# Kernel tuning notes

Hardware: AMD Instinct MI355X
Metric: run time of the kernel (lower is better)

Reference implementation:

```python
import jax, jax.numpy as jnp
import numpy as np
from jax import lax

C = 256
B, H, W = 8, 64, 64


def dwconv(x, w, b, pad):
    # x: [B,C,H,W], w: [C,1,kh,kw] depthwise (groups=C), b: [C]
    y = lax.conv_general_dilated(
        x, w,
        window_strides=(1, 1),
        padding=pad,
        dimension_numbers=('NCHW', 'OIHW', 'NCHW'),
        feature_group_count=x.shape[1],
    )
    return y + b[None, :, None, None]


def setup_inputs() -> dict:
    key = jax.random.key(0)
    ks = jax.random.split(key, 16)
    s = 0.05
    inp = {
        'x': jax.random.normal(ks[0], (B, C, H, W), jnp.float32),
        'w0':   jax.random.normal(ks[1], (C, 1, 5, 5), jnp.float32) * s,
        'b0':   jax.random.normal(ks[2], (C,), jnp.float32) * s,
        'w0_1': jax.random.normal(ks[3], (C, 1, 1, 7), jnp.float32) * s,
        'b0_1': jax.random.normal(ks[4], (C,), jnp.float32) * s,
        'w0_2': jax.random.normal(ks[5], (C, 1, 7, 1), jnp.float32) * s,
        'b0_2': jax.random.normal(ks[6], (C,), jnp.float32) * s,
        'w1_1': jax.random.normal(ks[7], (C, 1, 1, 11), jnp.float32) * s,
        'b1_1': jax.random.normal(ks[8], (C,), jnp.float32) * s,
        'w1_2': jax.random.normal(ks[9], (C, 1, 11, 1), jnp.float32) * s,
        'b1_2': jax.random.normal(ks[10], (C,), jnp.float32) * s,
        'w2_1': jax.random.normal(ks[11], (C, 1, 1, 21), jnp.float32) * s,
        'b2_1': jax.random.normal(ks[12], (C,), jnp.float32) * s,
        'w2_2': jax.random.normal(ks[13], (C, 1, 21, 1), jnp.float32) * s,
        'b2_2': jax.random.normal(ks[14], (C,), jnp.float32) * s,
    }
    return inp


def reference(x, w0, b0, w0_1, b0_1, w0_2, b0_2,
              w1_1, b1_1, w1_2, b1_2, w2_1, b2_1, w2_2, b2_2):
    # 5x5 depthwise, pad 2
    attn = dwconv(x, w0, b0, ((2, 2), (2, 2)))
    # stage 0: 1x7 / 7x1 strips
    a0x = dwconv(attn, w0_1, b0_1, ((0, 0), (3, 3)))
    a0y = dwconv(attn, w0_2, b0_2, ((3, 3), (0, 0)))
    attn_0 = a0x * a0y
    # stage 1: 1x11 / 11x1 strips
    a1x = dwconv(a0x, w1_1, b1_1, ((0, 0), (5, 5)))
    a1y = dwconv(a0y, w1_2, b1_2, ((5, 5), (0, 0)))
    attn_1 = a1x * a1y
    # stage 2: 1x21 / 21x1 strips
    a2x = dwconv(a1x, w2_1, b2_1, ((0, 0), (10, 10)))
    a2y = dwconv(a1y, w2_2, b2_2, ((10, 10), (0, 0)))
    attn_2 = a2x * a2y
    return (attn_0, attn_1, attn_2)
```

## Files before the change

### kernel.cpp

```cpp
#include <hip/hip_runtime.h>


#define RA_W 4624
#define RB_W 4352
#define LDS_WORDS (RA_W + RB_W)

typedef float v2f __attribute__((ext_vector_type(2)));

__device__ __forceinline__ float dpp_prev(float v) {
    return __int_as_float(__builtin_amdgcn_update_dpp(
        0, __float_as_int(v), 0x111, 0xF, 0xF, false));
}
__device__ __forceinline__ float dpp_next(float v) {
    return __int_as_float(__builtin_amdgcn_update_dpp(
        0, __float_as_int(v), 0x101, 0xF, 0xF, false));
}
__device__ __forceinline__ void ld4p(const float* p, v2f* w) {
    float4 q = *(const float4*)p;
    w[0].x = q.x; w[0].y = q.y; w[1].x = q.z; w[1].y = q.w;
}
__device__ __forceinline__ void st4p(float* p, v2f a, v2f b) {
    float4 q; q.x = a.x; q.y = a.y; q.z = b.x; q.w = b.y;
    *(float4*)p = q;
}
__device__ __forceinline__ float elem(const v2f* a, int e) {
    return (e & 1) ? a[e >> 1].y : a[e >> 1].x;
}

template<int K, int TAPOFF>
__device__ __forceinline__ void conv_acc(const float* __restrict__ wrow,
                                         const v2f* wnd, v2f* A) {
    #pragma unroll
    for (int v = 0; v < K; v++) {
        const float w = wrow[v];
        const int u = v + TAPOFF;
        if ((u & 1) == 0) {
            v2f wv; wv.x = w; wv.y = w;
            #pragma unroll
            for (int k = 0; k < 8; k++) A[k] += wv * wnd[(u >> 1) + k];
        } else {
            #pragma unroll
            for (int k = 0; k < 8; k++) {
                A[k].x += w * wnd[(u >> 1) + k].y;
                A[k].y += w * wnd[(u >> 1) + k + 1].x;
            }
        }
    }
}

template<int H>
__device__ __forceinline__ void build_twnd(const float* s, float* w, int jg) {
    float pv[H], nv[H];
    #pragma unroll
    for (int d = 0; d < H; d++) pv[d] = dpp_prev(s[16 - H + d]);
    #pragma unroll
    for (int d = 0; d < H; d++) nv[d] = dpp_next(s[d]);
    #pragma unroll
    for (int d = 0; d < H; d++) w[d] = jg ? pv[d] : 0.f;
    #pragma unroll
    for (int k = 0; k < 16; k++) w[H + k] = s[k];
    #pragma unroll
    for (int d = 0; d < H; d++) w[H + 16 + d] = (jg < 3) ? nv[d] : 0.f;
}
template<int K>
__device__ __forceinline__ void conv_t(const float* __restrict__ wrow,
                                       const float* w, float bb, float* acc) {
    #pragma unroll
    for (int k = 0; k < 16; k++) acc[k] = bb;
    #pragma unroll
    for (int u = 0; u < K; u++) {
        const float ww = wrow[u];
        #pragma unroll
        for (int k = 0; k < 16; k++) acc[k] += ww * w[k + u];
    }
}

__global__ __launch_bounds__(256, 4)
void msca_fused(const float* __restrict__ x,
                const float* __restrict__ w0,   const float* __restrict__ b0,
                const float* __restrict__ w0_1, const float* __restrict__ b0_1,
                const float* __restrict__ w0_2, const float* __restrict__ b0_2,
                const float* __restrict__ w1_1, const float* __restrict__ b1_1,
                const float* __restrict__ w1_2, const float* __restrict__ b1_2,
                const float* __restrict__ w2_1, const float* __restrict__ b2_1,
                const float* __restrict__ w2_2, const float* __restrict__ b2_2,
                float* __restrict__ out)
{
    __shared__ __align__(16) float lds[LDS_WORDS];
    float* RA = lds;
    float* RB = lds + RA_W;

    const int t  = threadIdx.x;
    const int r  = t >> 2;
    const int jg = t & 3;
    const int j0 = jg << 4;

    const int plane = blockIdx.x;
    const int ch    = plane & 255;

    const float* xg = x + (size_t)plane * 4096;
    float* o0 = out + (size_t)plane * 4096;
    float* o1 = o0 + 8388608;
    float* o2 = o1 + 8388608;

    v2f xR2[8];
    #pragma unroll
    for (int m = 0; m < 4; m++) ld4p(&xg[r * 64 + j0 + 4 * m], &xR2[2 * m]);

    #pragma unroll
    for (int k0 = 0; k0 < 2; k0++) {
        int k = t + 256 * k0;
        if (k < 272) RA[k < 136 ? k : k + 4352] = 0.f;
    }
    if (t < 64) {
        int b = (t + 2) * 68;
        RA[b] = 0.f; RA[b + 1] = 0.f; RA[b + 66] = 0.f; RA[b + 67] = 0.f;
    }
    {
        float* row = &RA[(r + 2) * 68];
        row[j0 + 2] = xR2[0].x;  row[j0 + 3] = xR2[0].y;
        st4p(&row[j0 + 4],  xR2[1], xR2[2]);
        st4p(&row[j0 + 8],  xR2[3], xR2[4]);
        st4p(&row[j0 + 12], xR2[5], xR2[6]);
        row[j0 + 16] = xR2[7].x; row[j0 + 17] = xR2[7].y;
    }
    __syncthreads();

    v2f attn2[8];
    {
        const float bb = b0[ch];
        #pragma unroll
        for (int k = 0; k < 8; k++) { attn2[k].x = bb; attn2[k].y = bb; }
        #pragma unroll
        for (int dr = 0; dr < 5; dr++) {
            v2f wnd[10];
            if (dr == 2) {
                float e0 = dpp_prev(xR2[7].x), e1 = dpp_prev(xR2[7].y);
                float n0 = dpp_next(xR2[0].x), n1 = dpp_next(xR2[0].y);
                wnd[0].x = jg ? e0 : 0.f;  wnd[0].y = jg ? e1 : 0.f;
                #pragma unroll
                for (int k = 0; k < 8; k++) wnd[1 + k] = xR2[k];
                wnd[9].x = (jg < 3) ? n0 : 0.f;  wnd[9].y = (jg < 3) ? n1 : 0.f;
            } else {
                const float* row = &RA[(r + dr) * 68 + j0];
                #pragma unroll
                for (int m = 0; m < 5; m++) ld4p(&row[4 * m], &wnd[2 * m]);
            }
            conv_acc<5, 0>(w0 + ch * 25 + dr * 5, wnd, attn2);
        }
        #pragma unroll
        for (int e = 0; e < 16; e++) RB[(j0 + e) * 68 + r] = elem(attn2, e);
    }
    __syncthreads();

    v2f a0x2[8];
    {
        const float bb = b0_1[ch];
        #pragma unroll
        for (int k = 0; k < 8; k++) { a0x2[k].x = bb; a0x2[k].y = bb; }
        v2f wnd[12];
        float p13 = dpp_prev(attn2[6].y), p14 = dpp_prev(attn2[7].x), p15 = dpp_prev(attn2[7].y);
        float n0 = dpp_next(attn2[0].x), n1 = dpp_next(attn2[0].y), n2 = dpp_next(attn2[1].x);
        wnd[0].x = 0.f;               wnd[0].y = jg ? p13 : 0.f;
        wnd[1].x = jg ? p14 : 0.f;    wnd[1].y = jg ? p15 : 0.f;
        #pragma unroll
        for (int k = 0; k < 8; k++) wnd[2 + k] = attn2[k];
        wnd[10].x = (jg < 3) ? n0 : 0.f;  wnd[10].y = (jg < 3) ? n1 : 0.f;
        wnd[11].x = (jg < 3) ? n2 : 0.f;  wnd[11].y = 0.f;
        conv_acc<7, 1>(w0_1 + ch * 7, wnd, a0x2);
    }
    float sT[16];
    #pragma unroll
    for (int m = 0; m < 4; m++) {
        float4 q = *(const float4*)&RB[r * 68 + j0 + 4 * m];
        sT[4 * m] = q.x; sT[4 * m + 1] = q.y; sT[4 * m + 2] = q.z; sT[4 * m + 3] = q.w;
    }
    float a0y[16];
    {
        float w[22];
        build_twnd<3>(sT, w, jg);
        conv_t<7>(w0_2 + ch * 7, w, b0_2[ch], a0y);
        #pragma unroll
        for (int e = 0; e < 16; e++) RA[(j0 + e) * 68 + r] = a0y[e];
    }
    __syncthreads();

    v2f prod0[8];
    #pragma unroll
    for (int m = 0; m < 4; m++) {
        v2f p[2]; ld4p(&RA[r * 68 + j0 + 4 * m], p);
        prod0[2 * m]     = a0x2[2 * m] * p[0];
        prod0[2 * m + 1] = a0x2[2 * m + 1] * p[1];
    }
    v2f a1x2[8];
    {
        const float bb = b1_1[ch];
        #pragma unroll
        for (int k = 0; k < 8; k++) { a1x2[k].x = bb; a1x2[k].y = bb; }
        v2f wnd[14];
        float p11 = dpp_prev(a0x2[5].y), p12 = dpp_prev(a0x2[6].x), p13 = dpp_prev(a0x2[6].y);
        float p14 = dpp_prev(a0x2[7].x), p15 = dpp_prev(a0x2[7].y);
        float n0 = dpp_next(a0x2[0].x), n1 = dpp_next(a0x2[0].y), n2 = dpp_next(a0x2[1].x);
        float n3 = dpp_next(a0x2[1].y), n4 = dpp_next(a0x2[2].x);
        wnd[0].x = 0.f;             wnd[0].y = jg ? p11 : 0.f;
        wnd[1].x = jg ? p12 : 0.f;  wnd[1].y = jg ? p13 : 0.f;
        wnd[2].x = jg ? p14 : 0.f;  wnd[2].y = jg ? p15 : 0.f;
        #pragma unroll
        for (int k = 0; k < 8; k++) wnd[3 + k] = a0x2[k];
        wnd[11].x = (jg < 3) ? n0 : 0.f;  wnd[11].y = (jg < 3) ? n1 : 0.f;
        wnd[12].x = (jg < 3) ? n2 : 0.f;  wnd[12].y = (jg < 3) ? n3 : 0.f;
        wnd[13].x = (jg < 3) ? n4 : 0.f;  wnd[13].y = 0.f;
        conv_acc<11, 1>(w1_1 + ch * 11, wnd, a1x2);
    }
    float a1y[16];
    {
        float w[26];
        build_twnd<5>(a0y, w, jg);
        conv_t<11>(w1_2 + ch * 11, w, b1_2[ch], a1y);
        #pragma unroll
        for (int e = 0; e < 16; e++) RB[(j0 + e) * 68 + r] = a1y[e];
    }
    __syncthreads();

    st4p(&o0[r * 64 + j0],      prod0[0], prod0[1]);
    st4p(&o0[r * 64 + j0 + 4],  prod0[2], prod0[3]);
    st4p(&o0[r * 64 + j0 + 8],  prod0[4], prod0[5]);
    st4p(&o0[r * 64 + j0 + 12], prod0[6], prod0[7]);

    v2f prod1[8];
    #pragma unroll
    for (int m = 0; m < 4; m++) {
        v2f p[2]; ld4p(&RB[r * 68 + j0 + 4 * m], p);
        prod1[2 * m]     = a1x2[2 * m] * p[0];
        prod1[2 * m + 1] = a1x2[2 * m + 1] * p[1];
    }
    v2f a2x2[8];
    {
        const float bb = b2_1[ch];
        #pragma unroll
        for (int k = 0; k < 8; k++) { a2x2[k].x = bb; a2x2[k].y = bb; }
        v2f wnd[18];
        float pv[10], nv[10];
        #pragma unroll
        for (int d = 0; d < 10; d++) {
            int q = 6 + d;
            float pe = dpp_prev((q & 1) ? a1x2[q >> 1].y : a1x2[q >> 1].x);
            float ne = dpp_next((d & 1) ? a1x2[d >> 1].y : a1x2[d >> 1].x);
            pv[d] = jg ? pe : 0.f;
            nv[d] = (jg < 3) ? ne : 0.f;
        }
        #pragma unroll
        for (int m = 0; m < 5; m++) { wnd[m].x = pv[2 * m]; wnd[m].y = pv[2 * m + 1]; }
        #pragma unroll
        for (int k = 0; k < 8; k++) wnd[5 + k] = a1x2[k];
        #pragma unroll
        for (int m = 0; m < 5; m++) { wnd[13 + m].x = nv[2 * m]; wnd[13 + m].y = nv[2 * m + 1]; }
        conv_acc<21, 0>(w2_1 + ch * 21, wnd, a2x2);
    }
    {
        float w[36], a2y[16];
        build_twnd<10>(a1y, w, jg);
        conv_t<21>(w2_2 + ch * 21, w, b2_2[ch], a2y);
        #pragma unroll
        for (int e = 0; e < 16; e++) RA[(j0 + e) * 68 + r] = a2y[e];
    }
    __syncthreads();

    st4p(&o1[r * 64 + j0],      prod1[0], prod1[1]);
    st4p(&o1[r * 64 + j0 + 4],  prod1[2], prod1[3]);
    st4p(&o1[r * 64 + j0 + 8],  prod1[4], prod1[5]);
    st4p(&o1[r * 64 + j0 + 12], prod1[6], prod1[7]);
    #pragma unroll
    for (int m = 0; m < 4; m++) {
        v2f p[2]; ld4p(&RA[r * 68 + j0 + 4 * m], p);
        v2f q0 = a2x2[2 * m] * p[0];
        v2f q1 = a2x2[2 * m + 1] * p[1];
        st4p(&o2[r * 64 + j0 + 4 * m], q0, q1);
    }
}

extern "C" void kernel_launch(void* const* d_in, const int* in_sizes, int n_in,
                              void* d_out, int out_size, void* d_ws, size_t ws_size,
                              hipStream_t stream) {
    msca_fused<<<2048, 256, 0, stream>>>(
        (const float*)d_in[0],
        (const float*)d_in[1],  (const float*)d_in[2],
        (const float*)d_in[3],  (const float*)d_in[4],
        (const float*)d_in[5],  (const float*)d_in[6],
        (const float*)d_in[7],  (const float*)d_in[8],
        (const float*)d_in[9],  (const float*)d_in[10],
        (const float*)d_in[11], (const float*)d_in[12],
        (const float*)d_in[13], (const float*)d_in[14],
        (float*)d_out);
}
```

Baseline: 47.22 us.

## Use 512 threads per plane with 8 columns each and swizzled LDS transposes

Each block now runs 512 threads, each owning 8 columns of a row instead of 16, which halves per-thread register state and raises the occupancy target. Horizontal strip halos are gathered with DPP row shifts by 1 and 2 lanes, since the 21-tap conv needs data from two neighbours. The transpose scatter and read now use an XOR swizzle to cut LDS bank conflicts. The packed v2f math is dropped in favour of scalar FMAs, which may give up dual-issue throughput.

After: 44.85 us. 1.05x faster.

```diff
diff --git a/kernel.cpp b/kernel.cpp
--- a/kernel.cpp
+++ b/kernel.cpp
@@ -5,77 +5,102 @@
 #define RB_W 4352
 #define LDS_WORDS (RA_W + RB_W)
 
-typedef float v2f __attribute__((ext_vector_type(2)));
-
-__device__ __forceinline__ float dpp_prev(float v) {
+__device__ __forceinline__ float dppsr1(float v) {
     return __int_as_float(__builtin_amdgcn_update_dpp(
         0, __float_as_int(v), 0x111, 0xF, 0xF, false));
 }
-__device__ __forceinline__ float dpp_next(float v) {
+__device__ __forceinline__ float dppsr2(float v) {
+    return __int_as_float(__builtin_amdgcn_update_dpp(
+        0, __float_as_int(v), 0x112, 0xF, 0xF, false));
+}
+__device__ __forceinline__ float dppsl1(float v) {
     return __int_as_float(__builtin_amdgcn_update_dpp(
         0, __float_as_int(v), 0x101, 0xF, 0xF, false));
 }
-__device__ __forceinline__ void ld4p(const float* p, v2f* w) {
-    float4 q = *(const float4*)p;
-    w[0].x = q.x; w[0].y = q.y; w[1].x = q.z; w[1].y = q.w;
-}
-__device__ __forceinline__ void st4p(float* p, v2f a, v2f b) {
-    float4 q; q.x = a.x; q.y = a.y; q.z = b.x; q.w = b.y;
-    *(float4*)p = q;
-}
-__device__ __forceinline__ float elem(const v2f* a, int e) {
-    return (e & 1) ? a[e >> 1].y : a[e >> 1].x;
-}
-
-template<int K, int TAPOFF>
-__device__ __forceinline__ void conv_acc(const float* __restrict__ wrow,
-                                         const v2f* wnd, v2f* A) {
+__device__ __forceinline__ float dppsl2(float v) {
+    return __int_as_float(__builtin_amdgcn_update_dpp(
+        0, __float_as_int(v), 0x102, 0xF, 0xF, false));
+}
+__device__ __forceinline__ void ld8(const float* p, float* d) {
+    float4 a = *(const float4*)p, b = *(const float4*)(p + 4);
+    d[0]=a.x; d[1]=a.y; d[2]=a.z; d[3]=a.w; d[4]=b.x; d[5]=b.y; d[6]=b.z; d[7]=b.w;
+}
+__device__ __forceinline__ void st8(float* p, const float* d) {
+    float4 a, b;
+    a.x=d[0]; a.y=d[1]; a.z=d[2]; a.w=d[3]; b.x=d[4]; b.y=d[5]; b.z=d[6]; b.w=d[7];
+    *(float4*)p = a; *(float4*)(p + 4) = b;
+}
+
+template<int K, int W0, int N>
+__device__ __forceinline__ void cpart(const float* __restrict__ wt,
+                                      const float* s, float* acc) {
     #pragma unroll
     for (int v = 0; v < K; v++) {
-        const float w = wrow[v];
-        const int u = v + TAPOFF;
-        if ((u & 1) == 0) {
-            v2f wv; wv.x = w; wv.y = w;
-            #pragma unroll
-            for (int k = 0; k < 8; k++) A[k] += wv * wnd[(u >> 1) + k];
-        } else {
-            #pragma unroll
-            for (int k = 0; k < 8; k++) {
-                A[k].x += w * wnd[(u >> 1) + k].y;
-                A[k].y += w * wnd[(u >> 1) + k + 1].x;
-            }
+        #pragma unroll
+        for (int j = 0; j < 8; j++) {
+            const int p = j + v - W0;
+            if (p >= 0 && p < N) acc[j] += wt[v] * s[p];
         }
     }
 }
 
 template<int H>
-__device__ __forceinline__ void build_twnd(const float* s, float* w, int jg) {
+__device__ __forceinline__ void sconv(const float* __restrict__ wt, float bb,
+                                      const float* a, bool pm, bool np, float* acc) {
+    constexpr int K = 2 * H + 1;
     float pv[H], nv[H];
     #pragma unroll
-    for (int d = 0; d < H; d++) pv[d] = dpp_prev(s[16 - H + d]);
-    #pragma unroll
-    for (int d = 0; d < H; d++) nv[d] = dpp_next(s[d]);
-    #pragma unroll
-    for (int d = 0; d < H; d++) w[d] = jg ? pv[d] : 0.f;
-    #pragma unroll
-    for (int k = 0; k < 16; k++) w[H + k] = s[k];
-    #pragma unroll
-    for (int d = 0; d < H; d++) w[H + 16 + d] = (jg < 3) ? nv[d] : 0.f;
-}
-template<int K>
-__device__ __forceinline__ void conv_t(const float* __restrict__ wrow,
-                                       const float* w, float bb, float* acc) {
-    #pragma unroll
-    for (int k = 0; k < 16; k++) acc[k] = bb;
-    #pragma unroll
-    for (int u = 0; u < K; u++) {
-        const float ww = wrow[u];
-        #pragma unroll
-        for (int k = 0; k < 16; k++) acc[k] += ww * w[k + u];
-    }
-}
-
-__global__ __launch_bounds__(256, 4)
+    for (int i = 0; i < H; i++) pv[i] = dppsr1(a[8 - H + i]);
+    #pragma unroll
+    for (int i = 0; i < H; i++) nv[i] = dppsl1(a[i]);
+    #pragma unroll
+    for (int i = 0; i < H; i++) pv[i] = pm ? pv[i] : 0.f;
+    #pragma unroll
+    for (int i = 0; i < H; i++) nv[i] = np ? nv[i] : 0.f;
+    #pragma unroll
+    for (int j = 0; j < 8; j++) acc[j] = bb;
+    cpart<K, 0, H>(wt, pv, acc);
+    cpart<K, H, 8>(wt, a, acc);
+    cpart<K, H + 8, H>(wt, nv, acc);
+}
+
+__device__ __forceinline__ void sconv21(const float* __restrict__ wt, float bb,
+                                        const float* a, bool pm, bool pm2,
+                                        bool np, bool np2, float* acc) {
+    #pragma unroll
+    for (int j = 0; j < 8; j++) acc[j] = bb;
+    {
+        float q[2];
+        q[0] = dppsr2(a[6]); q[1] = dppsr2(a[7]);
+        q[0] = pm2 ? q[0] : 0.f; q[1] = pm2 ? q[1] : 0.f;
+        cpart<21, 0, 2>(wt, q, acc);
+    }
+    {
+        float pv[8];
+        #pragma unroll
+        for (int i = 0; i < 8; i++) pv[i] = dppsr1(a[i]);
+        #pragma unroll
+        for (int i = 0; i < 8; i++) pv[i] = pm ? pv[i] : 0.f;
+        cpart<21, 2, 8>(wt, pv, acc);
+    }
+    cpart<21, 10, 8>(wt, a, acc);
+    {
+        float nv[8];
+        #pragma unroll
+        for (int i = 0; i < 8; i++) nv[i] = dppsl1(a[i]);
+        #pragma unroll
+        for (int i = 0; i < 8; i++) nv[i] = np ? nv[i] : 0.f;
+        cpart<21, 18, 8>(wt, nv, acc);
+    }
+    {
+        float q[2];
+        q[0] = dppsl2(a[0]); q[1] = dppsl2(a[1]);
+        q[0] = np2 ? q[0] : 0.f; q[1] = np2 ? q[1] : 0.f;
+        cpart<21, 26, 2>(wt, q, acc);
+    }
+}
+
+__global__ __launch_bounds__(512, 8)
 void msca_fused(const float* __restrict__ x,
                 const float* __restrict__ w0,   const float* __restrict__ b0,
                 const float* __restrict__ w0_1, const float* __restrict__ b0_1,
@@ -90,10 +115,16 @@
     float* RA = lds;
     float* RB = lds + RA_W;
 
-    const int t  = threadIdx.x;
-    const int r  = t >> 2;
-    const int jg = t & 3;
-    const int j0 = jg << 4;
+    const int t     = threadIdx.x;
+    const int maj   = t >> 3;
+    const int lane8 = t & 7;
+    const int j0    = lane8 << 3;
+
+    const bool pm  = lane8 >= 1, np  = lane8 <= 6;
+    const bool pm2 = lane8 >= 2, np2 = lane8 <= 5;
+
+    const int scat = maj ^ (lane8 << 3);
+    const int rdb  = maj * 68 + ((lane8 ^ ((maj >> 3) & 7)) << 3);
 
     const int plane = blockIdx.x;
     const int ch    = plane & 255;
@@ -103,186 +134,108 @@
     float* o1 = o0 + 8388608;
     float* o2 = o1 + 8388608;
 
-    v2f xR2[8];
-    #pragma unroll
-    for (int m = 0; m < 4; m++) ld4p(&xg[r * 64 + j0 + 4 * m], &xR2[2 * m]);
-
-    #pragma unroll
-    for (int k0 = 0; k0 < 2; k0++) {
-        int k = t + 256 * k0;
-        if (k < 272) RA[k < 136 ? k : k + 4352] = 0.f;
-    }
-    if (t < 64) {
-        int b = (t + 2) * 68;
-        RA[b] = 0.f; RA[b + 1] = 0.f; RA[b + 66] = 0.f; RA[b + 67] = 0.f;
-    }
-    {
-        float* row = &RA[(r + 2) * 68];
-        row[j0 + 2] = xR2[0].x;  row[j0 + 3] = xR2[0].y;
-        st4p(&row[j0 + 4],  xR2[1], xR2[2]);
-        st4p(&row[j0 + 8],  xR2[3], xR2[4]);
-        st4p(&row[j0 + 12], xR2[5], xR2[6]);
-        row[j0 + 16] = xR2[7].x; row[j0 + 17] = xR2[7].y;
-    }
-    __syncthreads();
-
-    v2f attn2[8];
+    float xr[8];
+    ld8(&xg[maj * 64 + j0], xr);
+    if (t < 136) { RA[t] = 0.f; RA[t + 4488] = 0.f; }
+    if (t < 256) {
+        int rr = 2 + (t >> 2), cc = t & 3;
+        RA[rr * 68 + (cc < 2 ? cc : cc + 64)] = 0.f;
+    }
+    {
+        float* row = &RA[(maj + 2) * 68 + j0 + 2];
+        float2 p;
+        p.x = xr[0]; p.y = xr[1]; ((float2*)row)[0] = p;
+        p.x = xr[2]; p.y = xr[3]; ((float2*)row)[1] = p;
+        p.x = xr[4]; p.y = xr[5]; ((float2*)row)[2] = p;
+        p.x = xr[6]; p.y = xr[7]; ((float2*)row)[3] = p;
+    }
+    __syncthreads();
+
+    float attn[8];
     {
         const float bb = b0[ch];
         #pragma unroll
-        for (int k = 0; k < 8; k++) { attn2[k].x = bb; attn2[k].y = bb; }
+        for (int j = 0; j < 8; j++) attn[j] = bb;
+        const float* w0p = w0 + ch * 25;
         #pragma unroll
         for (int dr = 0; dr < 5; dr++) {
-            v2f wnd[10];
-            if (dr == 2) {
-                float e0 = dpp_prev(xR2[7].x), e1 = dpp_prev(xR2[7].y);
-                float n0 = dpp_next(xR2[0].x), n1 = dpp_next(xR2[0].y);
-                wnd[0].x = jg ? e0 : 0.f;  wnd[0].y = jg ? e1 : 0.f;
+            float wnd[12];
+            const float* rowp = &RA[(maj + dr) * 68 + j0];
+            float4 qa = *(const float4*)rowp;
+            float4 qb = *(const float4*)(rowp + 4);
+            float4 qc = *(const float4*)(rowp + 8);
+            wnd[0]=qa.x; wnd[1]=qa.y; wnd[2]=qa.z;  wnd[3]=qa.w;
+            wnd[4]=qb.x; wnd[5]=qb.y; wnd[6]=qb.z;  wnd[7]=qb.w;
+            wnd[8]=qc.x; wnd[9]=qc.y; wnd[10]=qc.z; wnd[11]=qc.w;
+            #pragma unroll
+            for (int v = 0; v < 5; v++) {
+                const float ww = w0p[dr * 5 + v];
                 #pragma unroll
-                for (int k = 0; k < 8; k++) wnd[1 + k] = xR2[k];
-                wnd[9].x = (jg < 3) ? n0 : 0.f;  wnd[9].y = (jg < 3) ? n1 : 0.f;
-            } else {
-                const float* row = &RA[(r + dr) * 68 + j0];
-                #pragma unroll
-                for (int m = 0; m < 5; m++) ld4p(&row[4 * m], &wnd[2 * m]);
+                for (int j = 0; j < 8; j++) attn[j] += ww * wnd[j + v];
             }
-            conv_acc<5, 0>(w0 + ch * 25 + dr * 5, wnd, attn2);
         }
         #pragma unroll
-        for (int e = 0; e < 16; e++) RB[(j0 + e) * 68 + r] = elem(attn2, e);
-    }
-    __syncthreads();
-
-    v2f a0x2[8];
-    {
-        const float bb = b0_1[ch];
-        #pragma unroll
-        for (int k = 0; k < 8; k++) { a0x2[k].x = bb; a0x2[k].y = bb; }
-        v2f wnd[12];
-        float p13 = dpp_prev(attn2[6].y), p14 = dpp_prev(attn2[7].x), p15 = dpp_prev(attn2[7].y);
-        float n0 = dpp_next(attn2[0].x), n1 = dpp_next(attn2[0].y), n2 = dpp_next(attn2[1].x);
-        wnd[0].x = 0.f;               wnd[0].y = jg ? p13 : 0.f;
-        wnd[1].x = jg ? p14 : 0.f;    wnd[1].y = jg ? p15 : 0.f;
-        #pragma unroll
-        for (int k = 0; k < 8; k++) wnd[2 + k] = attn2[k];
-        wnd[10].x = (jg < 3) ? n0 : 0.f;  wnd[10].y = (jg < 3) ? n1 : 0.f;
-        wnd[11].x = (jg < 3) ? n2 : 0.f;  wnd[11].y = 0.f;
-        conv_acc<7, 1>(w0_1 + ch * 7, wnd, a0x2);
-    }
-    float sT[16];
-    #pragma unroll
-    for (int m = 0; m < 4; m++) {
-        float4 q = *(const float4*)&RB[r * 68 + j0 + 4 * m];
-        sT[4 * m] = q.x; sT[4 * m + 1] = q.y; sT[4 * m + 2] = q.z; sT[4 * m + 3] = q.w;
-    }
-    float a0y[16];
-    {
-        float w[22];
-        build_twnd<3>(sT, w, jg);
-        conv_t<7>(w0_2 + ch * 7, w, b0_2[ch], a0y);
-        #pragma unroll
-        for (int e = 0; e < 16; e++) RA[(j0 + e) * 68 + r] = a0y[e];
-    }
-    __syncthreads();
-
-    v2f prod0[8];
-    #pragma unroll
-    for (int m = 0; m < 4; m++) {
-        v2f p[2]; ld4p(&RA[r * 68 + j0 + 4 * m], p);
-        prod0[2 * m]     = a0x2[2 * m] * p[0];
-        prod0[2 * m + 1] = a0x2[2 * m + 1] * p[1];
-    }
-    v2f a1x2[8];
-    {
-        const float bb = b1_1[ch];
-        #pragma unroll
-        for (int k = 0; k < 8; k++) { a1x2[k].x = bb; a1x2[k].y = bb; }
-        v2f wnd[14];
-        float p11 = dpp_prev(a0x2[5].y), p12 = dpp_prev(a0x2[6].x), p13 = dpp_prev(a0x2[6].y);
-        float p14 = dpp_prev(a0x2[7].x), p15 = dpp_prev(a0x2[7].y);
-        float n0 = dpp_next(a0x2[0].x), n1 = dpp_next(a0x2[0].y), n2 = dpp_next(a0x2[1].x);
-        float n3 = dpp_next(a0x2[1].y), n4 = dpp_next(a0x2[2].x);
-        wnd[0].x = 0.f;             wnd[0].y = jg ? p11 : 0.f;
-        wnd[1].x = jg ? p12 : 0.f;  wnd[1].y = jg ? p13 : 0.f;
-        wnd[2].x = jg ? p14 : 0.f;  wnd[2].y = jg ? p15 : 0.f;
-        #pragma unroll
-        for (int k = 0; k < 8; k++) wnd[3 + k] = a0x2[k];
-        wnd[11].x = (jg < 3) ? n0 : 0.f;  wnd[11].y = (jg < 3) ? n1 : 0.f;
-        wnd[12].x = (jg < 3) ? n2 : 0.f;  wnd[12].y = (jg < 3) ? n3 : 0.f;
-        wnd[13].x = (jg < 3) ? n4 : 0.f;  wnd[13].y = 0.f;
-        conv_acc<11, 1>(w1_1 + ch * 11, wnd, a1x2);
-    }
-    float a1y[16];
-    {
-        float w[26];
-        build_twnd<5>(a0y, w, jg);
-        conv_t<11>(w1_2 + ch * 11, w, b1_2[ch], a1y);
-        #pragma unroll
-        for (int e = 0; e < 16; e++) RB[(j0 + e) * 68 + r] = a1y[e];
-    }
-    __syncthreads();
-
-    st4p(&o0[r * 64 + j0],      prod0[0], prod0[1]);
-    st4p(&o0[r * 64 + j0 + 4],  prod0[2], prod0[3]);
-    st4p(&o0[r * 64 + j0 + 8],  prod0[4], prod0[5]);
-    st4p(&o0[r * 64 + j0 + 12], prod0[6], prod0[7]);
-
-    v2f prod1[8];
-    #pragma unroll
-    for (int m = 0; m < 4; m++) {
-        v2f p[2]; ld4p(&RB[r * 68 + j0 + 4 * m], p);
-        prod1[2 * m]     = a1x2[2 * m] * p[0];
-        prod1[2 * m + 1] = a1x2[2 * m + 1] * p[1];
-    }
-    v2f a2x2[8];
-    {
-        const float bb = b2_1[ch];
-        #pragma unroll
-        for (int k = 0; k < 8; k++) { a2x2[k].x = bb; a2x2[k].y = bb; }
-        v2f wnd[18];
-        float pv[10], nv[10];
-        #pragma unroll
-        for (int d = 0; d < 10; d++) {
-            int q = 6 + d;
-            float pe = dpp_prev((q & 1) ? a1x2[q >> 1].y : a1x2[q >> 1].x);
-            float ne = dpp_next((d & 1) ? a1x2[d >> 1].y : a1x2[d >> 1].x);
-            pv[d] = jg ? pe : 0.f;
-            nv[d] = (jg < 3) ? ne : 0.f;
-        }
-        #pragma unroll
-        for (int m = 0; m < 5; m++) { wnd[m].x = pv[2 * m]; wnd[m].y = pv[2 * m + 1]; }
-        #pragma unroll
-        for (int k = 0; k < 8; k++) wnd[5 + k] = a1x2[k];
-        #pragma unroll
-        for (int m = 0; m < 5; m++) { wnd[13 + m].x = nv[2 * m]; wnd[13 + m].y = nv[2 * m + 1]; }
-        conv_acc<21, 0>(w2_1 + ch * 21, wnd, a2x2);
-    }
-    {
-        float w[36], a2y[16];
-        build_twnd<10>(a1y, w, jg);
-        conv_t<21>(w2_2 + ch * 21, w, b2_2[ch], a2y);
-        #pragma unroll
-        for (int e = 0; e < 16; e++) RA[(j0 + e) * 68 + r] = a2y[e];
-    }
-    __syncthreads();
-
-    st4p(&o1[r * 64 + j0],      prod1[0], prod1[1]);
-    st4p(&o1[r * 64 + j0 + 4],  prod1[2], prod1[3]);
-    st4p(&o1[r * 64 + j0 + 8],  prod1[4], prod1[5]);
-    st4p(&o1[r * 64 + j0 + 12], prod1[6], prod1[7]);
-    #pragma unroll
-    for (int m = 0; m < 4; m++) {
-        v2f p[2]; ld4p(&RA[r * 68 + j0 + 4 * m], p);
-        v2f q0 = a2x2[2 * m] * p[0];
-        v2f q1 = a2x2[2 * m + 1] * p[1];
-        st4p(&o2[r * 64 + j0 + 4 * m], q0, q1);
+        for (int e = 0; e < 8; e++) RB[(j0 + e) * 68 + scat] = attn[e];
+    }
+    __syncthreads();
+
+    float a0x[8];
+    sconv<3>(w0_1 + ch * 7, b0_1[ch], attn, pm, np, a0x);
+    float stv[8];
+    ld8(&RB[rdb], stv);
+    float aty0[8];
+    sconv<3>(w0_2 + ch * 7, b0_2[ch], stv, pm, np, aty0);
+    #pragma unroll
+    for (int d = 0; d < 8; d++) RA[(j0 + d) * 68 + scat] = aty0[d];
+    __syncthreads();
+
+    float prod0[8];
+    {
+        float y0r[8];
+        ld8(&RA[rdb], y0r);
+        #pragma unroll
+        for (int j = 0; j < 8; j++) prod0[j] = a0x[j] * y0r[j];
+    }
+    float a1x[8];
+    sconv<5>(w1_1 + ch * 11, b1_1[ch], a0x, pm, np, a1x);
+    float aty1[8];
+    sconv<5>(w1_2 + ch * 11, b1_2[ch], aty0, pm, np, aty1);
+    #pragma unroll
+    for (int d = 0; d < 8; d++) RB[(j0 + d) * 68 + scat] = aty1[d];
+    __syncthreads();
+
+    st8(&o0[maj * 64 + j0], prod0);
+    float prod1[8];
+    {
+        float y1r[8];
+        ld8(&RB[rdb], y1r);
+        #pragma unroll
+        for (int j = 0; j < 8; j++) prod1[j] = a1x[j] * y1r[j];
+    }
+    {
+        float a2y[8];
+        sconv21(w2_2 + ch * 21, b2_2[ch], aty1, pm, pm2, np, np2, a2y);
+        #pragma unroll
+        for (int d = 0; d < 8; d++) RA[(j0 + d) * 68 + scat] = a2y[d];
+    }
+    float a2x[8];
+    sconv21(w2_1 + ch * 21, b2_1[ch], a1x, pm, pm2, np, np2, a2x);
+    __syncthreads();
+
+    st8(&o1[maj * 64 + j0], prod1);
+    {
+        float y2r[8], prod2[8];
+        ld8(&RA[rdb], y2r);
+        #pragma unroll
+        for (int j = 0; j < 8; j++) prod2[j] = a2x[j] * y2r[j];
+        st8(&o2[maj * 64 + j0], prod2);
     }
 }
 
 extern "C" void kernel_launch(void* const* d_in, const int* in_sizes, int n_in,
                               void* d_out, int out_size, void* d_ws, size_t ws_size,
                               hipStream_t stream) {
-    msca_fused<<<2048, 256, 0, stream>>>(
+    msca_fused<<<2048, 512, 0, stream>>>(
         (const float*)d_in[0],
         (const float*)d_in[1],  (const float*)d_in[2],
         (const float*)d_in[3],  (const float*)d_in[4],
```
